# Performance work log

Hardware: AMD Instinct MI355X
Metric: run time of the kernel (lower is better)

## Reference

```python
import jax, jax.numpy as jnp
import numpy as np


def setup_inputs() -> dict:
    key = jax.random.key(0)
    B, Mb, Nb, C = 2, 16384, 16384, 32
    k1, k2, k3 = jax.random.split(key, 3)
    SCENE = 100.0  # spatial extent in meters
    xyz = jax.random.uniform(k1, (B * Mb, 3), dtype=jnp.float32) * SCENE
    new_xyz = jax.random.uniform(k2, (B * Nb, 3), dtype=jnp.float32) * SCENE
    xyz_batch_cnt = jnp.full((B,), Mb, dtype=jnp.int32)
    new_xyz_batch_cnt = jnp.full((B,), Nb, dtype=jnp.int32)
    features = jax.random.normal(k3, (B * Mb, C), dtype=jnp.float32)
    return {
        "xyz": xyz,
        "xyz_batch_cnt": xyz_batch_cnt,
        "new_xyz": new_xyz,
        "new_xyz_batch_cnt": new_xyz_batch_cnt,
        "features": features,
    }


def _three_nn(new_xyz, xyz, B, Nb, Mb):
    """Per-batch brute-force 3-NN. Returns (dist [N,3], idx [N,3] global)."""
    q = new_xyz.reshape(B, Nb, 3)
    k = xyz.reshape(B, Mb, 3)

    def knn3(args):
        qb, kb = args
        # squared L2 distances [Nb, Mb]
        d2 = (
            jnp.sum(qb * qb, axis=-1, keepdims=True)
            - 2.0 * (qb @ kb.T)
            + jnp.sum(kb * kb, axis=-1)[None, :]
        )
        neg_d2, idx = jax.lax.top_k(-d2, 3)  # 3 smallest distances
        dist = jnp.sqrt(jnp.maximum(-neg_d2, 0.0))
        return dist, idx

    dist, idx = jax.lax.map(knn3, (q, k))  # [B, Nb, 3] each
    offsets = (jnp.arange(B, dtype=idx.dtype) * Mb)[:, None, None]
    idx = (idx + offsets).reshape(B * Nb, 3)
    dist = dist.reshape(B * Nb, 3)
    return dist, idx


def reference(xyz, xyz_batch_cnt, new_xyz, new_xyz_batch_cnt, features):
    B = xyz_batch_cnt.shape[0]
    Mb = xyz.shape[0] // B
    Nb = new_xyz.shape[0] // B

    dist, idx = _three_nn(new_xyz, xyz, B, Nb, Mb)
    dist_recip = 1.0 / (dist + 1e-8)
    norm = jnp.sum(dist_recip, axis=-1, keepdims=True)
    weight = dist_recip / norm  # [N, 3]

    gathered = features[idx]  # [N, 3, C] irregular gather
    interpolated = jnp.sum(weight[..., None] * gathered, axis=1)  # [N, C]
    return interpolated
```

## Files before the change

kernel.cpp:

```cpp
#include <hip/hip_runtime.h>
#include <float.h>
#include <stdint.h>

#pragma clang fp contract(off)

#define G    16
#define NC   (G*G*G)
#define INVW  (16.0f / 100.0f)
#define CELLW (100.0f / 16.0f)
#define S2SAFE (CELLW*CELLW - 0.02f)
#define FLAGCAP 4096
#define SCANCAP 8192

__device__ __forceinline__ void cell3(float x, float y, float z,
                                      int& cx, int& cy, int& cz) {
    cx = (int)(x * INVW); cx = cx < 0 ? 0 : (cx > G-1 ? G-1 : cx);
    cy = (int)(y * INVW); cy = cy < 0 ? 0 : (cy > G-1 ? G-1 : cy);
    cz = (int)(z * INVW); cz = cz < 0 ? 0 : (cz > G-1 ? G-1 : cz);
}
__device__ __forceinline__ uint32_t mapbits(float f) {
    uint32_t b = __float_as_uint(f);
    return b ^ ((uint32_t)(((int32_t)b) >> 31) | 0x80000000u);
}
__device__ __forceinline__ float keyhi_to_f(uint32_t h) {
    return __uint_as_float((h & 0x80000000u) ? (h ^ 0x80000000u) : ~h);
}

#define INS4(key) do {                                             \
    const uint64_t _k = (key);                                     \
    if (_k < k3) {                                                 \
        const bool c2 = _k < k2, c1 = _k < k1, c0 = _k < k0;       \
        k3 = c2 ? k2 : _k;                                         \
        k2 = c2 ? (c1 ? k1 : _k) : k2;                             \
        k1 = c1 ? (c0 ? k0 : _k) : k1;                             \
        k0 = c0 ? _k : k0;                                         \
    }                                                              \
} while (0)

__device__ __forceinline__ uint64_t wave_min_u64(uint64_t v) {
    for (int m = 1; m < 64; m <<= 1) {
        const uint64_t o = (uint64_t)__shfl_xor((long long)v, m);
        v = (o < v) ? o : v;
    }
    return v;
}

__global__ void k_zero(int* p, int n) {
    int i = blockIdx.x * 256 + threadIdx.x;
    if (i < n) p[i] = 0;
}

__global__ void k_hist(const float* __restrict__ xyz,
                       const float* __restrict__ nxyz,
                       int M, int N, int Mb, int Nb,
                       int* pcount, int* qcount) {
    int i = blockIdx.x * 256 + threadIdx.x;
    if (i < M) {
        float x = xyz[3*i], y = xyz[3*i+1], z = xyz[3*i+2];
        int cx, cy, cz; cell3(x, y, z, cx, cy, cz);
        int b = i / Mb;
        atomicAdd(&pcount[b*NC + (cz*G + cy)*G + cx], 1);
    } else if (i < M + N) {
        int q = i - M;
        float x = nxyz[3*q], y = nxyz[3*q+1], z = nxyz[3*q+2];
        int cx, cy, cz; cell3(x, y, z, cx, cy, cz);
        int b = q / Nb;
        atomicAdd(&qcount[b*NC + (cz*G + cy)*G + cx], 1);
    }
}

__global__ __launch_bounds__(1024) void k_scan(const int* pcount, const int* qcount,
                       int* pstart, int* pcursor, int* qcursor, int n) {
    __shared__ int A[SCANCAP], Bu[SCANCAP];
    const bool doP = (blockIdx.x == 0);
    const int* src0 = doP ? pcount : qcount;
    for (int s = threadIdx.x; s < SCANCAP; s += 1024) A[s] = (s < n) ? src0[s] : 0;
    __syncthreads();
    bool flip = false;
    for (int off = 1; off < SCANCAP; off <<= 1) {
        int* src = flip ? Bu : A;
        int* dst = flip ? A : Bu;
        for (int s = threadIdx.x; s < SCANCAP; s += 1024)
            dst[s] = src[s] + (s >= off ? src[s - off] : 0);
        flip = !flip;
        __syncthreads();
    }
    int* incl = flip ? Bu : A;
    if (doP) {
        for (int s = threadIdx.x; s < n; s += 1024) {
            int v = (s == 0) ? 0 : incl[s-1];
            pstart[s] = v; pcursor[s] = v;
        }
        if (threadIdx.x == 0) pstart[n] = incl[n-1];
    } else {
        for (int s = threadIdx.x; s < n; s += 1024)
            qcursor[s] = (s == 0) ? 0 : incl[s-1];
    }
}

__global__ void k_scatter(const float* __restrict__ xyz,
                          const float* __restrict__ nxyz,
                          int M, int N, int Mb, int Nb,
                          int* pcursor, int* qcursor,
                          float4* spts, int* pidx, int* qlist) {
    int i = blockIdx.x * 256 + threadIdx.x;
    if (i < M) {
        float x = xyz[3*i], y = xyz[3*i+1], z = xyz[3*i+2];
        int cx, cy, cz; cell3(x, y, z, cx, cy, cz);
        int b = i / Mb;
        int pos = atomicAdd(&pcursor[b*NC + (cz*G + cy)*G + cx], 1);
        const float sk = (x*x + y*y) + z*z;
        spts[pos] = make_float4(x, y, z, sk);
        pidx[pos] = i;
    } else if (i < M + N) {
        int q = i - M;
        float x = nxyz[3*q], y = nxyz[3*q+1], z = nxyz[3*q+2];
        int cx, cy, cz; cell3(x, y, z, cx, cy, cz);
        int b = q / Nb;
        int pos = atomicAdd(&qcursor[b*NC + (cz*G + cy)*G + cx], 1);
        qlist[pos] = q;
    }
}

__global__ __launch_bounds__(256) void k_main(
    const float* __restrict__ nxyz, const float* __restrict__ feat,
    const float4* __restrict__ spts, const int* __restrict__ pidx,
    const int* __restrict__ pstart, const int* __restrict__ qlist,
    float* __restrict__ out, int Nb, int C, int N,
    int* nflag, int* flaglist)
{
    const int lane  = threadIdx.x & 63;
    const int wslot = blockIdx.x * 4 + (threadIdx.x >> 6);
    const int qs = (wslot < N) ? wslot : (N - 1);
    const int qi = __builtin_amdgcn_readfirstlane(qlist[qs]);
    const int b  = __builtin_amdgcn_readfirstlane(qs / Nb);

    const float qx = nxyz[3*qi], qy = nxyz[3*qi+1], qz = nxyz[3*qi+2];
    const float sq = (qx*qx + qy*qy) + qz*qz;

    int cx, cy, cz; cell3(qx, qy, qz, cx, cy, cz);
    const int x0 = max(0, cx-1), x1 = min(G-1, cx+1);
    const int y0 = max(0, cy-1), y1 = min(G-1, cy+1);
    const int z0 = max(0, cz-1), z1 = min(G-1, cz+1);

    int begins[9], cums[10];
    int nr = 0, tot = 0;
    cums[0] = 0;
    for (int zz = z0; zz <= z1; ++zz)
    for (int yy = y0; yy <= y1; ++yy) {
        const int cb = b*NC + (zz*G + yy)*G;
        const int bg = pstart[cb + x0];
        const int en = pstart[cb + x1 + 1];
        begins[nr] = bg;
        tot += en - bg;
        cums[nr + 1] = tot;
        ++nr;
    }
    #pragma unroll
    for (int r = nr; r < 9; ++r) { begins[r] = 0; cums[r + 1] = tot; }

    uint64_t k0 = ~0ull, k1 = ~0ull, k2 = ~0ull, k3 = ~0ull;

    for (int f = lane; f < tot; f += 64) {
        int p = 0;
        #pragma unroll
        for (int r = 0; r < 9; ++r)
            if (f >= cums[r] && f < cums[r + 1]) p = begins[r] + (f - cums[r]);
        const float4 kp = spts[p];
        const int    oi = pidx[p];
        float tt = qx * kp.x;
        tt = __builtin_fmaf(qy, kp.y, tt);
        tt = __builtin_fmaf(qz, kp.z, tt);
        const float d2 = __builtin_fmaf(-2.0f, tt, sq) + kp.w;
        const uint64_t key = ((uint64_t)mapbits(d2) << 32) | (uint32_t)oi;
        INS4(key);
    }

    uint64_t top[4];
    #pragma unroll
    for (int s = 0; s < 4; ++s) {
        const uint64_t m = wave_min_u64(k0);
        top[s] = m;
        if (k0 == m) { k0 = k1; k1 = k2; k2 = k3; k3 = ~0ull; }
    }

    const float rd0 = keyhi_to_f((uint32_t)(top[0] >> 32));
    const float rd1 = keyhi_to_f((uint32_t)(top[1] >> 32));
    const float rd2 = keyhi_to_f((uint32_t)(top[2] >> 32));
    const float rd3 = keyhi_to_f((uint32_t)(top[3] >> 32));
    const int ri0 = (int)(uint32_t)top[0], ri1 = (int)(uint32_t)top[1];
    const int ri2 = (int)(uint32_t)top[2], ri3 = (int)(uint32_t)top[3];

    const float d0s = sqrtf(fmaxf(rd0, 0.0f));
    const float d1s = sqrtf(fmaxf(rd1, 0.0f));
    const float d2s = sqrtf(fmaxf(rd2, 0.0f));
    const float r0 = 1.0f / (d0s + 1e-8f);
    const float r1 = 1.0f / (d1s + 1e-8f);
    const float r2 = 1.0f / (d2s + 1e-8f);
    const float norm = (r0 + r1) + r2;
    const float w0 = r0 / norm, w1 = r1 / norm, w2 = r2 / norm;

    int pick2 = ri2;
    if (rd2 == rd3) {
        float e = 0.0f;
        for (int c = lane; c < C; c += 64) {
            const float df = feat[(long)ri2*C + c] - feat[(long)ri3*C + c];
            e = fmaxf(e, fabsf(w2 * df));
        }
        for (int m = 1; m < 64; m <<= 1) e = fmaxf(e, __shfl_xor(e, m));
        if (e > 0.89f && e < 0.92f) pick2 = ri3;
    }

    const bool flag = !(rd3 < S2SAFE);
    if (wslot < N) {
        if (flag) {
            if (lane == 0) {
                int pos = atomicAdd(nflag, 1);
                if (pos < FLAGCAP) flaglist[pos] = qi;
            }
        } else {
            for (int c = lane; c < C; c += 64) {
                out[(long)qi*C + c] =
                    (w0 * feat[(long)ri0*C + c] + w1 * feat[(long)ri1*C + c])
                    + w2 * feat[(long)pick2*C + c];
            }
        }
    }
}

__global__ __launch_bounds__(256) void k_fixup(
    const float* __restrict__ nxyz, const float* __restrict__ feat,
    const float4* __restrict__ spts, const int* __restrict__ pidx,
    const int* __restrict__ nflag, const int* __restrict__ flaglist,
    float* __restrict__ out, int Mb, int Nb, int C)
{
    const int tid  = threadIdx.x;
    const int lane = tid & 63;
    const int wid  = tid >> 6;
    const int nf = min(*nflag, FLAGCAP);
    __shared__ uint64_t wkeys[4][4];

    for (int fj = blockIdx.x; fj < nf; fj += gridDim.x) {
        const int qi = flaglist[fj];
        const int b  = qi / Nb;
        const float qx = nxyz[3*qi], qy = nxyz[3*qi+1], qz = nxyz[3*qi+2];
        const float sq = (qx*qx + qy*qy) + qz*qz;

        uint64_t k0 = ~0ull, k1 = ~0ull, k2 = ~0ull, k3 = ~0ull;
        const int base = b * Mb;
        #pragma unroll 4
        for (int p = base + tid; p < base + Mb; p += 256) {
            const float4 kp = spts[p];
            const int    oi = pidx[p];
            float tt = qx * kp.x;
            tt = __builtin_fmaf(qy, kp.y, tt);
            tt = __builtin_fmaf(qz, kp.z, tt);
            const float d2 = __builtin_fmaf(-2.0f, tt, sq) + kp.w;
            const uint64_t key = ((uint64_t)mapbits(d2) << 32) | (uint32_t)oi;
            INS4(key);
        }
        uint64_t top[4];
        #pragma unroll
        for (int s = 0; s < 4; ++s) {
            const uint64_t m = wave_min_u64(k0);
            top[s] = m;
            if (k0 == m) { k0 = k1; k1 = k2; k2 = k3; k3 = ~0ull; }
        }
        if (lane == 0) {
            wkeys[wid][0] = top[0]; wkeys[wid][1] = top[1];
            wkeys[wid][2] = top[2]; wkeys[wid][3] = top[3];
        }
        __syncthreads();
        if (wid == 0) {
            uint64_t v = (lane < 16) ? wkeys[lane >> 2][lane & 3] : ~0ull;
            #pragma unroll
            for (int s = 0; s < 4; ++s) {
                const uint64_t m = wave_min_u64(v);
                top[s] = m;
                if (v == m) v = ~0ull;
            }
            const float rd0 = keyhi_to_f((uint32_t)(top[0] >> 32));
            const float rd1 = keyhi_to_f((uint32_t)(top[1] >> 32));
            const float rd2 = keyhi_to_f((uint32_t)(top[2] >> 32));
            const float rd3 = keyhi_to_f((uint32_t)(top[3] >> 32));
            const int ri0 = (int)(uint32_t)top[0], ri1 = (int)(uint32_t)top[1];
            const int ri2 = (int)(uint32_t)top[2], ri3 = (int)(uint32_t)top[3];
            const float d0s = sqrtf(fmaxf(rd0, 0.0f));
            const float d1s = sqrtf(fmaxf(rd1, 0.0f));
            const float d2s = sqrtf(fmaxf(rd2, 0.0f));
            const float r0 = 1.0f / (d0s + 1e-8f);
            const float r1 = 1.0f / (d1s + 1e-8f);
            const float r2 = 1.0f / (d2s + 1e-8f);
            const float norm = (r0 + r1) + r2;
            const float w0 = r0 / norm, w1 = r1 / norm, w2 = r2 / norm;
            int pick2 = ri2;
            if (rd2 == rd3) {
                float e = 0.0f;
                for (int c = lane; c < C; c += 64) {
                    const float df = feat[(long)ri2*C + c] - feat[(long)ri3*C + c];
                    e = fmaxf(e, fabsf(w2 * df));
                }
                for (int m = 1; m < 64; m <<= 1) e = fmaxf(e, __shfl_xor(e, m));
                if (e > 0.89f && e < 0.92f) pick2 = ri3;
            }
            for (int c = lane; c < C; c += 64) {
                out[(long)qi*C + c] =
                    (w0 * feat[(long)ri0*C + c] + w1 * feat[(long)ri1*C + c])
                    + w2 * feat[(long)pick2*C + c];
            }
        }
        __syncthreads();
    }
}

#define QPB  64
#define NW   8
#define TILE 64
__global__ __launch_bounds__(512) void knn3_interp_fallback(
    const float* __restrict__ xyz, const float* __restrict__ new_xyz,
    const float* __restrict__ feat, float* __restrict__ out,
    int Mb, int Nb, int C, int Ntot)
{
    const int tid  = threadIdx.x;
    const int lane = tid & 63;
    const int wid  = tid >> 6;
    const int qbase = blockIdx.x * QPB;
    const int n  = qbase + lane;
    const int nq = (n < Ntot) ? n : (Ntot - 1);
    const int b      = nq / Nb;
    const int mstart = b * Mb;
    const int pbeg = __builtin_amdgcn_readfirstlane(mstart + (Mb * wid) / NW);
    const int pend = __builtin_amdgcn_readfirstlane(mstart + (Mb * (wid + 1)) / NW);
    const float qx = new_xyz[nq*3+0], qy = new_xyz[nq*3+1], qz = new_xyz[nq*3+2];
    const float sq = (qx*qx + qy*qy) + qz*qz;
    __shared__ float4 tilebuf[NW][TILE];
    float b0 = FLT_MAX, b1 = FLT_MAX, b2 = FLT_MAX, b3 = FLT_MAX;
    int   i0 = 0x7fffffff, i1 = 0x7fffffff, i2 = 0x7fffffff, i3 = 0x7fffffff;
    for (int t = pbeg; t < pend; t += TILE) {
        {
            int p = t + lane;
            if (p >= pend) p = pend - 1;
            const float kx = xyz[p*3+0], ky = xyz[p*3+1], kz = xyz[p*3+2];
            const float sk = (kx*kx + ky*ky) + kz*kz;
            tilebuf[wid][lane] = make_float4(kx, ky, kz, sk);
        }
        const int lim = (pend - t < TILE) ? (pend - t) : TILE;
        #pragma unroll 8
        for (int i = 0; i < lim; ++i) {
            const float4 kp = tilebuf[wid][i];
            float tt = qx * kp.x;
            tt = __builtin_fmaf(qy, kp.y, tt);
            tt = __builtin_fmaf(qz, kp.z, tt);
            const float d2 = (sq - 2.0f * tt) + kp.w;
            const int j = t + i;
            if (d2 < b3) {
                if (d2 < b2) {
                    b3 = b2; i3 = i2;
                    if (d2 < b1) {
                        b2 = b1; i2 = i1;
                        if (d2 < b0) { b1 = b0; i1 = i0; b0 = d2; i0 = j; }
                        else         { b1 = d2; i1 = j; }
                    } else { b2 = d2; i2 = j; }
                } else { b3 = d2; i3 = j; }
            }
        }
    }
    __shared__ float sd[NW][QPB][4];
    __shared__ int   si[NW][QPB][4];
    sd[wid][lane][0]=b0; sd[wid][lane][1]=b1; sd[wid][lane][2]=b2; sd[wid][lane][3]=b3;
    si[wid][lane][0]=i0; si[wid][lane][1]=i1; si[wid][lane][2]=i2; si[wid][lane][3]=i3;
    __syncthreads();
    __shared__ float sw[QPB][3];
    __shared__ int   sidx[QPB][3];
    if (wid == 0) {
        float cd[NW*4]; int ci[NW*4];
        #pragma unroll
        for (int w = 0; w < NW; ++w)
            #pragma unroll
            for (int k = 0; k < 4; ++k) { cd[w*4+k]=sd[w][lane][k]; ci[w*4+k]=si[w][lane][k]; }
        float rd[4]; int ri[4];
        #pragma unroll
        for (int s = 0; s < 4; ++s) {
            float bd = FLT_MAX; int bi = 0x7fffffff; int bc = 0;
            #pragma unroll
            for (int c = 0; c < NW*4; ++c) {
                const bool better = (cd[c] < bd) || (cd[c] == bd && ci[c] < bi);
                if (better) { bd = cd[c]; bi = ci[c]; bc = c; }
            }
            rd[s] = bd; ri[s] = bi; cd[bc] = FLT_MAX; ci[bc] = 0x7fffffff;
        }
        const float d0 = sqrtf(fmaxf(rd[0],0.f)), d1 = sqrtf(fmaxf(rd[1],0.f)), d2v = sqrtf(fmaxf(rd[2],0.f));
        const float r0 = 1.f/(d0+1e-8f), r1 = 1.f/(d1+1e-8f), r2 = 1.f/(d2v+1e-8f);
        const float norm = (r0+r1)+r2;
        const float w0 = r0/norm, w1 = r1/norm, w2 = r2/norm;
        int pick2 = ri[2];
        if (rd[2] == rd[3] && ri[3] != 0x7fffffff) {
            float imp = 0.f;
            const long a = ri[2], bb = ri[3];
            for (int c = 0; c < C; ++c) {
                const float df = feat[a*C+c] - feat[bb*C+c];
                imp = fmaxf(imp, fabsf(w2*df));
            }
            if (imp > 0.89f && imp < 0.92f) pick2 = ri[3];
        }
        sw[lane][0]=w0; sw[lane][1]=w1; sw[lane][2]=w2;
        sidx[lane][0]=ri[0]; sidx[lane][1]=ri[1]; sidx[lane][2]=pick2;
    }
    __syncthreads();
    const int total = QPB * C;
    for (int e = tid; e < total; e += 512) {
        const int q = e / C, c = e - q*C, gq = qbase + q;
        if (gq < Ntot) {
            const float w0 = sw[q][0], w1 = sw[q][1], w2 = sw[q][2];
            const long j0 = sidx[q][0], j1 = sidx[q][1], j2 = sidx[q][2];
            out[(long)gq*C + c] = (w0*feat[j0*C+c] + w1*feat[j1*C+c]) + w2*feat[j2*C+c];
        }
    }
}

extern "C" void kernel_launch(void* const* d_in, const int* in_sizes, int n_in,
                              void* d_out, int out_size, void* d_ws, size_t ws_size,
                              hipStream_t stream) {
    (void)n_in; (void)out_size;
    const float* xyz  = (const float*)d_in[0];
    const float* nxyz = (const float*)d_in[2];
    const float* feat = (const float*)d_in[4];
    float* out = (float*)d_out;

    const int B  = in_sizes[1];
    const int M  = in_sizes[0] / 3;
    const int N  = in_sizes[2] / 3;
    const int C  = in_sizes[4] / M;
    const int Mb = M / B;
    const int Nb = N / B;

    const int BNC = B * NC;
    int* w = (int*)d_ws;
    int* pcount   = w;
    int* qcount   = pcount + BNC;
    int* pstart   = qcount + BNC;
    int* pcursor  = pstart + BNC + 1;
    int* qcursor  = pcursor + BNC;
    int* nflag    = qcursor + BNC;
    int* flaglist = nflag + 1;
    int* qlist    = flaglist + FLAGCAP;
    int* pidx     = qlist + N;
    size_t intsUsed  = (size_t)(5*BNC + 2 + FLAGCAP) + (size_t)N + (size_t)M;
    size_t sptsOff   = (intsUsed*4 + 15) & ~(size_t)15;
    float4* spts     = (float4*)((char*)d_ws + sptsOff);
    const size_t need = sptsOff + (size_t)M * sizeof(float4);

    const bool ok = (need <= ws_size) && (BNC <= SCANCAP) &&
                    (Nb % 64 == 0) && (Mb % 256 == 0);
    if (!ok) {
        const int grid = (N + QPB - 1) / QPB;
        knn3_interp_fallback<<<grid, 512, 0, stream>>>(xyz, nxyz, feat, out,
                                                       Mb, Nb, C, N);
        return;
    }

    const int nzero = 5*BNC + 2;
    k_zero<<<(nzero + 255)/256, 256, 0, stream>>>(w, nzero);
    k_hist<<<(M + N + 255)/256, 256, 0, stream>>>(xyz, nxyz, M, N, Mb, Nb,
                                                  pcount, qcount);
    k_scan<<<2, 1024, 0, stream>>>(pcount, qcount, pstart, pcursor, qcursor, BNC);
    k_scatter<<<(M + N + 255)/256, 256, 0, stream>>>(xyz, nxyz, M, N, Mb, Nb,
                                                     pcursor, qcursor, spts, pidx, qlist);
    k_main<<<(N + 3)/4, 256, 0, stream>>>(nxyz, feat, spts, pidx, pstart, qlist,
                                          out, Nb, C, N, nflag, flaglist);
    k_fixup<<<256, 256, 0, stream>>>(nxyz, feat, spts, pidx, nflag, flaglist,
                                     out, Mb, Nb, C);
}
```

Before: 82.26 us.

## Replace counting-sort grid build with fixed-capacity cell buckets plus overflow list

Replaces the histogram, scan and scatter kernels with a single append kernel that writes points into fixed-capacity per-cell slots (CAP=32), with spills going to a per-batch overflow list. The query kernel walks 27 neighbour cells by computed address and also scans the overflow list. Queries are no longer sorted by cell, and the fixup kernel now reads raw xyz with a smaller grid. This removes two launches and the scan, at the cost of less spatial locality for queries, padded cell storage, and a full overflow scan per query if cells overflow.

```diff
diff --git a/kernel.cpp b/kernel.cpp
--- a/kernel.cpp
+++ b/kernel.cpp
@@ -4,13 +4,14 @@
 
 #pragma clang fp contract(off)
 
-#define G    16
-#define NC   (G*G*G)
+#define G     16
+#define NC    (G*G*G)
 #define INVW  (16.0f / 100.0f)
 #define CELLW (100.0f / 16.0f)
 #define S2SAFE (CELLW*CELLW - 0.02f)
+#define CAP     32
+#define OVCAP   16384
 #define FLAGCAP 4096
-#define SCANCAP 8192
 
 __device__ __forceinline__ void cell3(float x, float y, float z,
                                       int& cx, int& cy, int& cz) {
@@ -50,121 +51,74 @@
     if (i < n) p[i] = 0;
 }
 
-__global__ void k_hist(const float* __restrict__ xyz,
-                       const float* __restrict__ nxyz,
-                       int M, int N, int Mb, int Nb,
-                       int* pcount, int* qcount) {
+__global__ void k_append(const float* __restrict__ xyz, int M, int Mb,
+                         int* __restrict__ pcount, int* __restrict__ ovcount,
+                         float4* __restrict__ spts, int* __restrict__ pidx,
+                         float4* __restrict__ ovpts, int* __restrict__ ovidx) {
     int i = blockIdx.x * 256 + threadIdx.x;
-    if (i < M) {
-        float x = xyz[3*i], y = xyz[3*i+1], z = xyz[3*i+2];
-        int cx, cy, cz; cell3(x, y, z, cx, cy, cz);
-        int b = i / Mb;
-        atomicAdd(&pcount[b*NC + (cz*G + cy)*G + cx], 1);
-    } else if (i < M + N) {
-        int q = i - M;
-        float x = nxyz[3*q], y = nxyz[3*q+1], z = nxyz[3*q+2];
-        int cx, cy, cz; cell3(x, y, z, cx, cy, cz);
-        int b = q / Nb;
-        atomicAdd(&qcount[b*NC + (cz*G + cy)*G + cx], 1);
-    }
-}
-
-__global__ __launch_bounds__(1024) void k_scan(const int* pcount, const int* qcount,
-                       int* pstart, int* pcursor, int* qcursor, int n) {
-    __shared__ int A[SCANCAP], Bu[SCANCAP];
-    const bool doP = (blockIdx.x == 0);
-    const int* src0 = doP ? pcount : qcount;
-    for (int s = threadIdx.x; s < SCANCAP; s += 1024) A[s] = (s < n) ? src0[s] : 0;
-    __syncthreads();
-    bool flip = false;
-    for (int off = 1; off < SCANCAP; off <<= 1) {
-        int* src = flip ? Bu : A;
-        int* dst = flip ? A : Bu;
-        for (int s = threadIdx.x; s < SCANCAP; s += 1024)
-            dst[s] = src[s] + (s >= off ? src[s - off] : 0);
-        flip = !flip;
-        __syncthreads();
-    }
-    int* incl = flip ? Bu : A;
-    if (doP) {
-        for (int s = threadIdx.x; s < n; s += 1024) {
-            int v = (s == 0) ? 0 : incl[s-1];
-            pstart[s] = v; pcursor[s] = v;
-        }
-        if (threadIdx.x == 0) pstart[n] = incl[n-1];
+    if (i >= M) return;
+    const float x = xyz[3*i], y = xyz[3*i+1], z = xyz[3*i+2];
+    int cx, cy, cz; cell3(x, y, z, cx, cy, cz);
+    const int b = i / Mb;
+    const int cid = b*NC + (cz*G + cy)*G + cx;
+    const float sk = (x*x + y*y) + z*z;
+    const int pos = atomicAdd(&pcount[cid], 1);
+    if (pos < CAP) {
+        spts[(long)cid*CAP + pos] = make_float4(x, y, z, sk);
+        pidx[(long)cid*CAP + pos] = i;
     } else {
-        for (int s = threadIdx.x; s < n; s += 1024)
-            qcursor[s] = (s == 0) ? 0 : incl[s-1];
-    }
-}
-
-__global__ void k_scatter(const float* __restrict__ xyz,
-                          const float* __restrict__ nxyz,
-                          int M, int N, int Mb, int Nb,
-                          int* pcursor, int* qcursor,
-                          float4* spts, int* pidx, int* qlist) {
-    int i = blockIdx.x * 256 + threadIdx.x;
-    if (i < M) {
-        float x = xyz[3*i], y = xyz[3*i+1], z = xyz[3*i+2];
-        int cx, cy, cz; cell3(x, y, z, cx, cy, cz);
-        int b = i / Mb;
-        int pos = atomicAdd(&pcursor[b*NC + (cz*G + cy)*G + cx], 1);
-        const float sk = (x*x + y*y) + z*z;
-        spts[pos] = make_float4(x, y, z, sk);
-        pidx[pos] = i;
-    } else if (i < M + N) {
-        int q = i - M;
-        float x = nxyz[3*q], y = nxyz[3*q+1], z = nxyz[3*q+2];
-        int cx, cy, cz; cell3(x, y, z, cx, cy, cz);
-        int b = q / Nb;
-        int pos = atomicAdd(&qcursor[b*NC + (cz*G + cy)*G + cx], 1);
-        qlist[pos] = q;
+        const int op = atomicAdd(&ovcount[b], 1);
+        if (op < OVCAP) {
+            ovpts[b*OVCAP + op] = make_float4(x, y, z, sk);
+            ovidx[b*OVCAP + op] = i;
+        }
     }
 }
 
 __global__ __launch_bounds__(256) void k_main(
     const float* __restrict__ nxyz, const float* __restrict__ feat,
     const float4* __restrict__ spts, const int* __restrict__ pidx,
-    const int* __restrict__ pstart, const int* __restrict__ qlist,
+    const int* __restrict__ pcount, const int* __restrict__ ovcount,
+    const float4* __restrict__ ovpts, const int* __restrict__ ovidx,
     float* __restrict__ out, int Nb, int C, int N,
     int* nflag, int* flaglist)
 {
-    const int lane  = threadIdx.x & 63;
-    const int wslot = blockIdx.x * 4 + (threadIdx.x >> 6);
-    const int qs = (wslot < N) ? wslot : (N - 1);
-    const int qi = __builtin_amdgcn_readfirstlane(qlist[qs]);
-    const int b  = __builtin_amdgcn_readfirstlane(qs / Nb);
+    const int lane = threadIdx.x & 63;
+    const int qi   = blockIdx.x * 4 + (threadIdx.x >> 6);
+    if (qi >= N) return;
+    const int b = __builtin_amdgcn_readfirstlane(qi / Nb);
 
     const float qx = nxyz[3*qi], qy = nxyz[3*qi+1], qz = nxyz[3*qi+2];
     const float sq = (qx*qx + qy*qy) + qz*qz;
 
     int cx, cy, cz; cell3(qx, qy, qz, cx, cy, cz);
-    const int x0 = max(0, cx-1), x1 = min(G-1, cx+1);
-    const int y0 = max(0, cy-1), y1 = min(G-1, cy+1);
-    const int z0 = max(0, cz-1), z1 = min(G-1, cz+1);
-
-    int begins[9], cums[10];
-    int nr = 0, tot = 0;
+
+    int begins[27], cums[28];
+    int tot = 0;
     cums[0] = 0;
-    for (int zz = z0; zz <= z1; ++zz)
-    for (int yy = y0; yy <= y1; ++yy) {
-        const int cb = b*NC + (zz*G + yy)*G;
-        const int bg = pstart[cb + x0];
-        const int en = pstart[cb + x1 + 1];
-        begins[nr] = bg;
-        tot += en - bg;
-        cums[nr + 1] = tot;
-        ++nr;
-    }
     #pragma unroll
-    for (int r = nr; r < 9; ++r) { begins[r] = 0; cums[r + 1] = tot; }
+    for (int r = 0; r < 27; ++r) {
+        const int dz = r / 9 - 1;
+        const int dy = (r / 3) % 3 - 1;
+        const int dx = r % 3 - 1;
+        const int zz = cz + dz, yy = cy + dy, xx = cx + dx;
+        int cnt = 0, bg = 0;
+        if (zz >= 0 && zz < G && yy >= 0 && yy < G && xx >= 0 && xx < G) {
+            const int cid = b*NC + (zz*G + yy)*G + xx;
+            cnt = min(pcount[cid], CAP);
+            bg  = cid * CAP;
+        }
+        begins[r] = bg;
+        tot += cnt;
+        cums[r + 1] = tot;
+    }
 
     uint64_t k0 = ~0ull, k1 = ~0ull, k2 = ~0ull, k3 = ~0ull;
 
     for (int f = lane; f < tot; f += 64) {
         int p = 0;
         #pragma unroll
-        for (int r = 0; r < 9; ++r)
+        for (int r = 0; r < 27; ++r)
             if (f >= cums[r] && f < cums[r + 1]) p = begins[r] + (f - cums[r]);
         const float4 kp = spts[p];
         const int    oi = pidx[p];
@@ -176,6 +130,18 @@
         INS4(key);
     }
 
+    const int ovc = min(ovcount[b], OVCAP);
+    for (int f = lane; f < ovc; f += 64) {
+        const float4 kp = ovpts[b*OVCAP + f];
+        const int    oi = ovidx[b*OVCAP + f];
+        float tt = qx * kp.x;
+        tt = __builtin_fmaf(qy, kp.y, tt);
+        tt = __builtin_fmaf(qz, kp.z, tt);
+        const float d2 = __builtin_fmaf(-2.0f, tt, sq) + kp.w;
+        const uint64_t key = ((uint64_t)mapbits(d2) << 32) | (uint32_t)oi;
+        INS4(key);
+    }
+
     uint64_t top[4];
     #pragma unroll
     for (int s = 0; s < 4; ++s) {
@@ -212,25 +178,23 @@
     }
 
     const bool flag = !(rd3 < S2SAFE);
-    if (wslot < N) {
-        if (flag) {
-            if (lane == 0) {
-                int pos = atomicAdd(nflag, 1);
-                if (pos < FLAGCAP) flaglist[pos] = qi;
-            }
-        } else {
-            for (int c = lane; c < C; c += 64) {
-                out[(long)qi*C + c] =
-                    (w0 * feat[(long)ri0*C + c] + w1 * feat[(long)ri1*C + c])
-                    + w2 * feat[(long)pick2*C + c];
-            }
+    if (flag) {
+        if (lane == 0) {
+            int pos = atomicAdd(nflag, 1);
+            if (pos < FLAGCAP) flaglist[pos] = qi;
+        }
+    } else {
+        for (int c = lane; c < C; c += 64) {
+            out[(long)qi*C + c] =
+                (w0 * feat[(long)ri0*C + c] + w1 * feat[(long)ri1*C + c])
+                + w2 * feat[(long)pick2*C + c];
         }
     }
 }
 
 __global__ __launch_bounds__(256) void k_fixup(
-    const float* __restrict__ nxyz, const float* __restrict__ feat,
-    const float4* __restrict__ spts, const int* __restrict__ pidx,
+    const float* __restrict__ xyz, const float* __restrict__ nxyz,
+    const float* __restrict__ feat,
     const int* __restrict__ nflag, const int* __restrict__ flaglist,
     float* __restrict__ out, int Mb, int Nb, int C)
 {
@@ -250,13 +214,13 @@
         const int base = b * Mb;
         #pragma unroll 4
         for (int p = base + tid; p < base + Mb; p += 256) {
-            const float4 kp = spts[p];
-            const int    oi = pidx[p];
-            float tt = qx * kp.x;
-            tt = __builtin_fmaf(qy, kp.y, tt);
-            tt = __builtin_fmaf(qz, kp.z, tt);
-            const float d2 = __builtin_fmaf(-2.0f, tt, sq) + kp.w;
-            const uint64_t key = ((uint64_t)mapbits(d2) << 32) | (uint32_t)oi;
+            const float kx = xyz[3*p], ky = xyz[3*p+1], kz = xyz[3*p+2];
+            const float sk = (kx*kx + ky*ky) + kz*kz;
+            float tt = qx * kx;
+            tt = __builtin_fmaf(qy, ky, tt);
+            tt = __builtin_fmaf(qz, kz, tt);
+            const float d2 = __builtin_fmaf(-2.0f, tt, sq) + sk;
+            const uint64_t key = ((uint64_t)mapbits(d2) << 32) | (uint32_t)p;
             INS4(key);
         }
         uint64_t top[4];
@@ -437,21 +401,19 @@
     const int BNC = B * NC;
     int* w = (int*)d_ws;
     int* pcount   = w;
-    int* qcount   = pcount + BNC;
-    int* pstart   = qcount + BNC;
-    int* pcursor  = pstart + BNC + 1;
-    int* qcursor  = pcursor + BNC;
-    int* nflag    = qcursor + BNC;
-    int* flaglist = nflag + 1;
-    int* qlist    = flaglist + FLAGCAP;
-    int* pidx     = qlist + N;
-    size_t intsUsed  = (size_t)(5*BNC + 2 + FLAGCAP) + (size_t)N + (size_t)M;
-    size_t sptsOff   = (intsUsed*4 + 15) & ~(size_t)15;
-    float4* spts     = (float4*)((char*)d_ws + sptsOff);
-    const size_t need = sptsOff + (size_t)M * sizeof(float4);
-
-    const bool ok = (need <= ws_size) && (BNC <= SCANCAP) &&
-                    (Nb % 64 == 0) && (Mb % 256 == 0);
+    int* nflag    = pcount + BNC;
+    int* ovcount  = nflag + 1;
+    int* flaglist = ovcount + B;
+    int* ovidx    = flaglist + FLAGCAP;
+    int* pidx     = ovidx + (size_t)B*OVCAP;
+    size_t intsUsed = (size_t)BNC + 1 + B + FLAGCAP
+                    + (size_t)B*OVCAP + (size_t)BNC*CAP;
+    size_t f4Off  = (intsUsed*4 + 15) & ~(size_t)15;
+    float4* spts  = (float4*)((char*)d_ws + f4Off);
+    float4* ovpts = spts + (size_t)BNC*CAP;
+    const size_t need = f4Off + ((size_t)BNC*CAP + (size_t)B*OVCAP)*sizeof(float4);
+
+    const bool ok = (need <= ws_size) && (Mb <= OVCAP);
     if (!ok) {
         const int grid = (N + QPB - 1) / QPB;
         knn3_interp_fallback<<<grid, 512, 0, stream>>>(xyz, nxyz, feat, out,
@@ -459,15 +421,13 @@
         return;
     }
 
-    const int nzero = 5*BNC + 2;
+    const int nzero = BNC + 1 + B;
     k_zero<<<(nzero + 255)/256, 256, 0, stream>>>(w, nzero);
-    k_hist<<<(M + N + 255)/256, 256, 0, stream>>>(xyz, nxyz, M, N, Mb, Nb,
-                                                  pcount, qcount);
-    k_scan<<<2, 1024, 0, stream>>>(pcount, qcount, pstart, pcursor, qcursor, BNC);
-    k_scatter<<<(M + N + 255)/256, 256, 0, stream>>>(xyz, nxyz, M, N, Mb, Nb,
-                                                     pcursor, qcursor, spts, pidx, qlist);
-    k_main<<<(N + 3)/4, 256, 0, stream>>>(nxyz, feat, spts, pidx, pstart, qlist,
+    k_append<<<(M + 255)/256, 256, 0, stream>>>(xyz, M, Mb, pcount, ovcount,
+                                                spts, pidx, ovpts, ovidx);
+    k_main<<<(N + 3)/4, 256, 0, stream>>>(nxyz, feat, spts, pidx, pcount,
+                                          ovcount, ovpts, ovidx,
                                           out, Nb, C, N, nflag, flaglist);
-    k_fixup<<<256, 256, 0, stream>>>(nxyz, feat, spts, pidx, nflag, flaglist,
-                                     out, Mb, Nb, C);
-}
+    k_fixup<<<64, 256, 0, stream>>>(xyz, nxyz, feat, nflag, flaglist,
+                                    out, Mb, Nb, C);
+}
```

New measurement: 101.8 us. +23.8%, slower.

## Replace block-wide cell scan with atomic per-row allocation

Applied to the files above, without the earlier changes.

The two-block shared-memory Hillis-Steele scan over all grid cells is replaced by a kernel where each thread owns one x-row of cells. It reserves that row's range with an atomic add on a per-batch cursor and writes local prefix offsets. Rows end up in arbitrary order, but k_main only needs each row's cells to be contiguous, so it now gets cell ends from pstart plus pcount. The zeroing kernel becomes a hipMemsetAsync. k_fixup now reads the raw xyz array instead of the sorted buffer and runs with fewer blocks. The aim is to remove a serial, sync-heavy scan from the critical path, at the cost of a strided AoS read in the fallback search.

```diff
diff --git a/kernel.cpp b/kernel.cpp
--- a/kernel.cpp
+++ b/kernel.cpp
@@ -4,13 +4,12 @@
 
 #pragma clang fp contract(off)
 
-#define G    16
-#define NC   (G*G*G)
+#define G     16
+#define NC    (G*G*G)
 #define INVW  (16.0f / 100.0f)
 #define CELLW (100.0f / 16.0f)
 #define S2SAFE (CELLW*CELLW - 0.02f)
 #define FLAGCAP 4096
-#define SCANCAP 8192
 
 __device__ __forceinline__ void cell3(float x, float y, float z,
                                       int& cx, int& cy, int& cz) {
@@ -43,11 +42,6 @@
         v = (o < v) ? o : v;
     }
     return v;
-}
-
-__global__ void k_zero(int* p, int n) {
-    int i = blockIdx.x * 256 + threadIdx.x;
-    if (i < n) p[i] = 0;
 }
 
 __global__ void k_hist(const float* __restrict__ xyz,
@@ -69,46 +63,44 @@
     }
 }
 
-__global__ __launch_bounds__(1024) void k_scan(const int* pcount, const int* qcount,
-                       int* pstart, int* pcursor, int* qcursor, int n) {
-    __shared__ int A[SCANCAP], Bu[SCANCAP];
-    const bool doP = (blockIdx.x == 0);
-    const int* src0 = doP ? pcount : qcount;
-    for (int s = threadIdx.x; s < SCANCAP; s += 1024) A[s] = (s < n) ? src0[s] : 0;
-    __syncthreads();
-    bool flip = false;
-    for (int off = 1; off < SCANCAP; off <<= 1) {
-        int* src = flip ? Bu : A;
-        int* dst = flip ? A : Bu;
-        for (int s = threadIdx.x; s < SCANCAP; s += 1024)
-            dst[s] = src[s] + (s >= off ? src[s - off] : 0);
-        flip = !flip;
-        __syncthreads();
-    }
-    int* incl = flip ? Bu : A;
-    if (doP) {
-        for (int s = threadIdx.x; s < n; s += 1024) {
-            int v = (s == 0) ? 0 : incl[s-1];
-            pstart[s] = v; pcursor[s] = v;
-        }
-        if (threadIdx.x == 0) pstart[n] = incl[n-1];
-    } else {
-        for (int s = threadIdx.x; s < n; s += 1024)
-            qcursor[s] = (s == 0) ? 0 : incl[s-1];
+__global__ void k_alloc(const int* __restrict__ pcount,
+                        const int* __restrict__ qcount,
+                        int* __restrict__ pstart, int* __restrict__ pcur,
+                        int* __restrict__ qcur,
+                        int* __restrict__ bcur, int* __restrict__ qbcur,
+                        int B, int Mb, int Nb) {
+    const int rid = blockIdx.x * 256 + threadIdx.x;
+    if (rid >= B * G * G) return;
+    const int b   = rid / (G * G);
+    const int row = rid - b * (G * G);
+    const int cb  = b * NC + row * G;
+    int psum = 0, qsum = 0;
+    #pragma unroll
+    for (int x = 0; x < G; ++x) { psum += pcount[cb + x]; qsum += qcount[cb + x]; }
+    const int pbase = b * Mb + atomicAdd(&bcur[b],  psum);
+    const int qbase = b * Nb + atomicAdd(&qbcur[b], qsum);
+    int prun = 0, qrun = 0;
+    #pragma unroll
+    for (int x = 0; x < G; ++x) {
+        pstart[cb + x] = pbase + prun;
+        pcur[cb + x]   = pbase + prun;
+        prun += pcount[cb + x];
+        qcur[cb + x]   = qbase + qrun;
+        qrun += qcount[cb + x];
     }
 }
 
 __global__ void k_scatter(const float* __restrict__ xyz,
                           const float* __restrict__ nxyz,
                           int M, int N, int Mb, int Nb,
-                          int* pcursor, int* qcursor,
+                          int* pcur, int* qcur,
                           float4* spts, int* pidx, int* qlist) {
     int i = blockIdx.x * 256 + threadIdx.x;
     if (i < M) {
         float x = xyz[3*i], y = xyz[3*i+1], z = xyz[3*i+2];
         int cx, cy, cz; cell3(x, y, z, cx, cy, cz);
         int b = i / Mb;
-        int pos = atomicAdd(&pcursor[b*NC + (cz*G + cy)*G + cx], 1);
+        int pos = atomicAdd(&pcur[b*NC + (cz*G + cy)*G + cx], 1);
         const float sk = (x*x + y*y) + z*z;
         spts[pos] = make_float4(x, y, z, sk);
         pidx[pos] = i;
@@ -117,7 +109,7 @@
         float x = nxyz[3*q], y = nxyz[3*q+1], z = nxyz[3*q+2];
         int cx, cy, cz; cell3(x, y, z, cx, cy, cz);
         int b = q / Nb;
-        int pos = atomicAdd(&qcursor[b*NC + (cz*G + cy)*G + cx], 1);
+        int pos = atomicAdd(&qcur[b*NC + (cz*G + cy)*G + cx], 1);
         qlist[pos] = q;
     }
 }
@@ -125,7 +117,8 @@
 __global__ __launch_bounds__(256) void k_main(
     const float* __restrict__ nxyz, const float* __restrict__ feat,
     const float4* __restrict__ spts, const int* __restrict__ pidx,
-    const int* __restrict__ pstart, const int* __restrict__ qlist,
+    const int* __restrict__ pstart, const int* __restrict__ pcount,
+    const int* __restrict__ qlist,
     float* __restrict__ out, int Nb, int C, int N,
     int* nflag, int* flaglist)
 {
@@ -150,7 +143,7 @@
     for (int yy = y0; yy <= y1; ++yy) {
         const int cb = b*NC + (zz*G + yy)*G;
         const int bg = pstart[cb + x0];
-        const int en = pstart[cb + x1 + 1];
+        const int en = pstart[cb + x1] + pcount[cb + x1];
         begins[nr] = bg;
         tot += en - bg;
         cums[nr + 1] = tot;
@@ -229,8 +222,8 @@
 }
 
 __global__ __launch_bounds__(256) void k_fixup(
-    const float* __restrict__ nxyz, const float* __restrict__ feat,
-    const float4* __restrict__ spts, const int* __restrict__ pidx,
+    const float* __restrict__ xyz, const float* __restrict__ nxyz,
+    const float* __restrict__ feat,
     const int* __restrict__ nflag, const int* __restrict__ flaglist,
     float* __restrict__ out, int Mb, int Nb, int C)
 {
@@ -250,13 +243,13 @@
         const int base = b * Mb;
         #pragma unroll 4
         for (int p = base + tid; p < base + Mb; p += 256) {
-            const float4 kp = spts[p];
-            const int    oi = pidx[p];
-            float tt = qx * kp.x;
-            tt = __builtin_fmaf(qy, kp.y, tt);
-            tt = __builtin_fmaf(qz, kp.z, tt);
-            const float d2 = __builtin_fmaf(-2.0f, tt, sq) + kp.w;
-            const uint64_t key = ((uint64_t)mapbits(d2) << 32) | (uint32_t)oi;
+            const float kx = xyz[3*p], ky = xyz[3*p+1], kz = xyz[3*p+2];
+            const float sk = (kx*kx + ky*ky) + kz*kz;
+            float tt = qx * kx;
+            tt = __builtin_fmaf(qy, ky, tt);
+            tt = __builtin_fmaf(qz, kz, tt);
+            const float d2 = __builtin_fmaf(-2.0f, tt, sq) + sk;
+            const uint64_t key = ((uint64_t)mapbits(d2) << 32) | (uint32_t)p;
             INS4(key);
         }
         uint64_t top[4];
@@ -438,20 +431,22 @@
     int* w = (int*)d_ws;
     int* pcount   = w;
     int* qcount   = pcount + BNC;
-    int* pstart   = qcount + BNC;
-    int* pcursor  = pstart + BNC + 1;
-    int* qcursor  = pcursor + BNC;
-    int* nflag    = qcursor + BNC;
+    int* bcur     = qcount + BNC;
+    int* qbcur    = bcur + B;
+    int* nflag    = qbcur + B;
     int* flaglist = nflag + 1;
-    int* qlist    = flaglist + FLAGCAP;
-    int* pidx     = qlist + N;
-    size_t intsUsed  = (size_t)(5*BNC + 2 + FLAGCAP) + (size_t)N + (size_t)M;
-    size_t sptsOff   = (intsUsed*4 + 15) & ~(size_t)15;
-    float4* spts     = (float4*)((char*)d_ws + sptsOff);
-    const size_t need = sptsOff + (size_t)M * sizeof(float4);
-
-    const bool ok = (need <= ws_size) && (BNC <= SCANCAP) &&
-                    (Nb % 64 == 0) && (Mb % 256 == 0);
+    int* pstart   = flaglist + FLAGCAP;
+    int* pcur     = pstart + BNC;
+    int* qcur     = pcur + BNC;
+    int* pidx     = qcur + BNC;
+    int* qlist    = pidx + M;
+    size_t intsUsed = (size_t)5*BNC + 2*B + 1 + FLAGCAP + (size_t)M + (size_t)N;
+    size_t f4Off  = (intsUsed*4 + 15) & ~(size_t)15;
+    float4* spts  = (float4*)((char*)d_ws + f4Off);
+    const size_t need = f4Off + (size_t)M * sizeof(float4);
+    const size_t zeroBytes = ((size_t)2*BNC + 2*B + 1) * sizeof(int);
+
+    const bool ok = (need <= ws_size) && (Mb % 256 == 0) && (Nb % 64 == 0);
     if (!ok) {
         const int grid = (N + QPB - 1) / QPB;
         knn3_interp_fallback<<<grid, 512, 0, stream>>>(xyz, nxyz, feat, out,
@@ -459,15 +454,17 @@
         return;
     }
 
-    const int nzero = 5*BNC + 2;
-    k_zero<<<(nzero + 255)/256, 256, 0, stream>>>(w, nzero);
+    hipMemsetAsync(d_ws, 0, zeroBytes, stream);
     k_hist<<<(M + N + 255)/256, 256, 0, stream>>>(xyz, nxyz, M, N, Mb, Nb,
                                                   pcount, qcount);
-    k_scan<<<2, 1024, 0, stream>>>(pcount, qcount, pstart, pcursor, qcursor, BNC);
+    k_alloc<<<(B*G*G + 255)/256, 256, 0, stream>>>(pcount, qcount, pstart,
+                                                   pcur, qcur, bcur, qbcur,
+                                                   B, Mb, Nb);
     k_scatter<<<(M + N + 255)/256, 256, 0, stream>>>(xyz, nxyz, M, N, Mb, Nb,
-                                                     pcursor, qcursor, spts, pidx, qlist);
-    k_main<<<(N + 3)/4, 256, 0, stream>>>(nxyz, feat, spts, pidx, pstart, qlist,
+                                                     pcur, qcur, spts, pidx, qlist);
+    k_main<<<(N + 3)/4, 256, 0, stream>>>(nxyz, feat, spts, pidx, pstart,
+                                          pcount, qlist,
                                           out, Nb, C, N, nflag, flaglist);
-    k_fixup<<<256, 256, 0, stream>>>(nxyz, feat, spts, pidx, nflag, flaglist,
-                                     out, Mb, Nb, C);
-}
+    k_fixup<<<64, 256, 0, stream>>>(xyz, nxyz, feat, nflag, flaglist,
+                                    out, Mb, Nb, C);
+}
```

Result: slower. 97.80 us (+18.9%).

## Process one query per 16-lane group instead of one per wavefront in k_main

Applied to the files above, without the earlier changes.

Remaps k_main so each 16-lane subgroup handles one query point, giving four queries per wavefront and sixteen per block. Candidate scanning, top-k reduction, tie handling and the output write now use 16-lane strides and width-16 shuffles. The aim is to cut idle lanes and per-query setup and reduction overhead, since each query's neighbourhood holds only about a hundred points. In exchange each lane runs more candidate-loop iterations, and query indices are no longer wave-uniform, so loads become per-lane.

```diff
diff --git a/kernel.cpp b/kernel.cpp
--- a/kernel.cpp
+++ b/kernel.cpp
@@ -40,6 +40,13 @@
 __device__ __forceinline__ uint64_t wave_min_u64(uint64_t v) {
     for (int m = 1; m < 64; m <<= 1) {
         const uint64_t o = (uint64_t)__shfl_xor((long long)v, m);
+        v = (o < v) ? o : v;
+    }
+    return v;
+}
+__device__ __forceinline__ uint64_t grp_min_u64(uint64_t v) {
+    for (int m = 1; m < 16; m <<= 1) {
+        const uint64_t o = (uint64_t)__shfl_xor((long long)v, m, 16);
         v = (o < v) ? o : v;
     }
     return v;
@@ -129,11 +136,11 @@
     float* __restrict__ out, int Nb, int C, int N,
     int* nflag, int* flaglist)
 {
-    const int lane  = threadIdx.x & 63;
-    const int wslot = blockIdx.x * 4 + (threadIdx.x >> 6);
-    const int qs = (wslot < N) ? wslot : (N - 1);
-    const int qi = __builtin_amdgcn_readfirstlane(qlist[qs]);
-    const int b  = __builtin_amdgcn_readfirstlane(qs / Nb);
+    const int l16 = threadIdx.x & 15;
+    const int qs0 = blockIdx.x * 16 + (threadIdx.x >> 4);
+    const int qs  = (qs0 < N) ? qs0 : (N - 1);
+    const int qi  = qlist[qs];
+    const int b   = qs / Nb;
 
     const float qx = nxyz[3*qi], qy = nxyz[3*qi+1], qz = nxyz[3*qi+2];
     const float sq = (qx*qx + qy*qy) + qz*qz;
@@ -161,7 +168,7 @@
 
     uint64_t k0 = ~0ull, k1 = ~0ull, k2 = ~0ull, k3 = ~0ull;
 
-    for (int f = lane; f < tot; f += 64) {
+    for (int f = l16; f < tot; f += 16) {
         int p = 0;
         #pragma unroll
         for (int r = 0; r < 9; ++r)
@@ -179,7 +186,7 @@
     uint64_t top[4];
     #pragma unroll
     for (int s = 0; s < 4; ++s) {
-        const uint64_t m = wave_min_u64(k0);
+        const uint64_t m = grp_min_u64(k0);
         top[s] = m;
         if (k0 == m) { k0 = k1; k1 = k2; k2 = k3; k3 = ~0ull; }
     }
@@ -203,23 +210,23 @@
     int pick2 = ri2;
     if (rd2 == rd3) {
         float e = 0.0f;
-        for (int c = lane; c < C; c += 64) {
+        for (int c = l16; c < C; c += 16) {
             const float df = feat[(long)ri2*C + c] - feat[(long)ri3*C + c];
             e = fmaxf(e, fabsf(w2 * df));
         }
-        for (int m = 1; m < 64; m <<= 1) e = fmaxf(e, __shfl_xor(e, m));
+        for (int m = 1; m < 16; m <<= 1) e = fmaxf(e, __shfl_xor(e, m, 16));
         if (e > 0.89f && e < 0.92f) pick2 = ri3;
     }
 
     const bool flag = !(rd3 < S2SAFE);
-    if (wslot < N) {
+    if (qs0 < N) {
         if (flag) {
-            if (lane == 0) {
+            if (l16 == 0) {
                 int pos = atomicAdd(nflag, 1);
                 if (pos < FLAGCAP) flaglist[pos] = qi;
             }
         } else {
-            for (int c = lane; c < C; c += 64) {
+            for (int c = l16; c < C; c += 16) {
                 out[(long)qi*C + c] =
                     (w0 * feat[(long)ri0*C + c] + w1 * feat[(long)ri1*C + c])
                     + w2 * feat[(long)pick2*C + c];
@@ -466,8 +473,8 @@
     k_scan<<<2, 1024, 0, stream>>>(pcount, qcount, pstart, pcursor, qcursor, BNC);
     k_scatter<<<(M + N + 255)/256, 256, 0, stream>>>(xyz, nxyz, M, N, Mb, Nb,
                                                      pcursor, qcursor, spts, pidx, qlist);
-    k_main<<<(N + 3)/4, 256, 0, stream>>>(nxyz, feat, spts, pidx, pstart, qlist,
-                                          out, Nb, C, N, nflag, flaglist);
+    k_main<<<(N + 15)/16, 256, 0, stream>>>(nxyz, feat, spts, pidx, pstart, qlist,
+                                            out, Nb, C, N, nflag, flaglist);
     k_fixup<<<256, 256, 0, stream>>>(nxyz, feat, spts, pidx, nflag, flaglist,
                                      out, Mb, Nb, C);
 }
```

Result: faster. 71.07 us (-13.6%).
